# Performance work log

Measured on AMD Instinct MI355X. Metric: run time of the kernel, lower is better.

The kernel has to match this reference:

```python
import jax, jax.numpy as jnp
import numpy as np

B, TE, TD, D = 32, 2048, 64, 1024

def setup_inputs() -> dict:
    key = jax.random.key(0)
    k1, k2, k3, k4, k5 = jax.random.split(key, 5)
    return {
        "encoder_outputs": jax.random.normal(k1, (B, TE, D), dtype=jnp.float32),
        "decoder_outputs": jax.random.normal(k2, (B, TD, D), dtype=jnp.float32),
        "W_a": jax.random.normal(k3, (D, D), dtype=jnp.float32) * (1.0 / np.sqrt(D)),
        "U_a": jax.random.normal(k4, (D, D), dtype=jnp.float32) * (1.0 / np.sqrt(D)),
        "V_a": jax.random.normal(k5, (D, 1), dtype=jnp.float32) * (1.0 / np.sqrt(D)),
    }

def reference(encoder_outputs, decoder_outputs, W_a, U_a, V_a):
    # Bahdanau additive attention over encoder positions, query = last decoder step.
    dec_last = decoder_outputs[:, -1, :]                      # [B, D]
    enc_W = jnp.einsum('bte,ef->btf', encoder_outputs, W_a)   # [B, Te, D]
    dec_U = jnp.einsum('bd,df->bf', dec_last, U_a)            # [B, D] (broadcast over Te instead of tile)
    tanh_out = jnp.tanh(enc_W + dec_U[:, None, :])            # [B, Te, D]
    scores = jnp.einsum('btf,fo->bt', tanh_out, V_a[:, 0:1])  # [B, Te] (squeeze of [B,Te,1])
    weights = jax.nn.softmax(scores, axis=1)                  # [B, Te]
    context = jnp.einsum('bte,bt->be', encoder_outputs, weights)  # [B, D]
    return context, weights[..., None]
```

## Files before the change

kernel.cpp:

```cpp
#include <hip/hip_runtime.h>
#include <stdint.h>

typedef __attribute__((ext_vector_type(8))) __bf16 bf16x8;
typedef __attribute__((ext_vector_type(4))) float  f32x4;

__device__ __forceinline__ uint16_t f2b(float f) {
  uint32_t u = __float_as_uint(f);
  u += 0x7fffu + ((u >> 16) & 1u);
  return (uint16_t)(u >> 16);
}
__device__ __forceinline__ float b2f_lo(uint32_t p) { return __uint_as_float(p << 16); }
__device__ __forceinline__ float b2f_hi(uint32_t p) { return __uint_as_float(p & 0xffff0000u); }

__device__ __forceinline__ float tanh_fast(float x) {
  float e = __expf(2.0f * x);
  return 1.0f - 2.0f / (e + 1.0f);
}

__device__ __forceinline__ void barrier_lgkm() {
  asm volatile("s_waitcnt lgkmcnt(0)\n\ts_barrier" ::: "memory");
}

__global__ __launch_bounds__(256) void convert_enc(const float4* __restrict__ in,
                                                   uint4* __restrict__ out) {
  int i = blockIdx.x * 256 + threadIdx.x;
  float4 a = in[2 * i], b = in[2 * i + 1];
  uint4 o;
  o.x = (uint32_t)f2b(a.x) | ((uint32_t)f2b(a.y) << 16);
  o.y = (uint32_t)f2b(a.z) | ((uint32_t)f2b(a.w) << 16);
  o.z = (uint32_t)f2b(b.x) | ((uint32_t)f2b(b.y) << 16);
  o.w = (uint32_t)f2b(b.z) | ((uint32_t)f2b(b.w) << 16);
  out[i] = o;
}

__global__ __launch_bounds__(256) void convert_WT(const float* __restrict__ W,
                                                  uint16_t* __restrict__ WT) {
  __shared__ float tile[64][65];
  int k0 = (blockIdx.x & 15) * 64;
  int n0 = (blockIdx.x >> 4) * 64;
  #pragma unroll
  for (int it = 0; it < 16; ++it) {
    int idx = it * 256 + threadIdx.x;
    int kr = idx >> 6, nc = idx & 63;
    tile[kr][nc] = W[(size_t)(k0 + kr) * 1024 + n0 + nc];
  }
  __syncthreads();
  #pragma unroll
  for (int it = 0; it < 16; ++it) {
    int idx = it * 256 + threadIdx.x;
    int nr = idx >> 6, kc = idx & 63;
    WT[(size_t)(n0 + nr) * 1024 + k0 + kc] = f2b(tile[kc][nr]);
  }
}

__global__ __launch_bounds__(256) void compute_u(const float* __restrict__ dec,
                                                 const float4* __restrict__ U4,
                                                 float* __restrict__ u) {
  int b = blockIdx.x >> 3, dseg = blockIdx.x & 7;
  __shared__ float sdec[128];
  if (threadIdx.x < 128)
    sdec[threadIdx.x] = dec[(size_t)b * 64 * 1024 + 63 * 1024 + dseg * 128 + threadIdx.x];
  __syncthreads();
  float4 a = {0.f, 0.f, 0.f, 0.f};
  const float4* Ub = U4 + (size_t)dseg * 128 * 256 + threadIdx.x;
  #pragma unroll 4
  for (int d = 0; d < 128; ++d) {
    float4 w = Ub[(size_t)d * 256];
    float s = sdec[d];
    a.x = fmaf(s, w.x, a.x);
    a.y = fmaf(s, w.y, a.y);
    a.z = fmaf(s, w.z, a.z);
    a.w = fmaf(s, w.w, a.w);
  }
  float* up = u + b * 1024 + threadIdx.x * 4;
  atomicAdd(up + 0, a.x);
  atomicAdd(up + 1, a.y);
  atomicAdd(up + 2, a.z);
  atomicAdd(up + 3, a.w);
}

__global__ __launch_bounds__(256, 3) void gemm_score(const uint16_t* __restrict__ A,
                                                     const uint16_t* __restrict__ BT,
                                                     const float* __restrict__ u,
                                                     const float* __restrict__ v,
                                                     float* __restrict__ spart) {
  __shared__ uint4 sAB[2][1024];
  __shared__ float sred[128];

  int bx = blockIdx.x;
  int g = bx >> 6, r = bx & 63;
  int mtile = g * 8 + (r & 7);
  int ntile = r >> 3;

  int tid = threadIdx.x;
  int lane = tid & 63;
  int wid  = tid >> 6;
  int wm = (wid & 1) * 64;
  int wn = (wid >> 1) * 64;
  int quad = lane >> 4, nib = lane & 15;
  const int lsw = lane ^ ((lane >> 4) << 1);

  f32x4 acc[4][4];
  #pragma unroll
  for (int i = 0; i < 4; ++i)
    #pragma unroll
    for (int j = 0; j < 4; ++j) acc[i][j] = (f32x4){0.f, 0.f, 0.f, 0.f};

  const int rowA = mtile * 128;
  const int rowB = ntile * 128;
  const int c0 = tid, c1 = tid + 256;
  const uint4* pA0 = (const uint4*)(A  + (size_t)(rowA + (c0 >> 2)) * 1024 + (c0 & 3) * 8);
  const uint4* pA1 = (const uint4*)(A  + (size_t)(rowA + (c1 >> 2)) * 1024 + (c1 & 3) * 8);
  const uint4* pB0 = (const uint4*)(BT + (size_t)(rowB + (c0 >> 2)) * 1024 + (c0 & 3) * 8);
  const uint4* pB1 = (const uint4*)(BT + (size_t)(rowB + (c1 >> 2)) * 1024 + (c1 & 3) * 8);
  const int s0 = (((c0 >> 6) << 6) | ((c0 & 3) << 4) | ((c0 >> 2) & 15)) ^ ((c0 & 3) << 1);
  const int s1 = (((c1 >> 6) << 6) | ((c1 & 3) << 4) | ((c1 >> 2) & 15)) ^ ((c1 & 3) << 1);

  uint4 A0a, A1a, B0a, B1a, A0b, A1b, B0b, B1b;

#define GEMM_STEP(BUF)                                                          \
  do {                                                                          \
    bf16x8 af[4], bf[4];                                                        \
    _Pragma("unroll")                                                           \
    for (int i = 0; i < 4; ++i)                                                 \
      af[i] = *(const bf16x8*)&sAB[BUF][((wm >> 4) + i) * 64 + lsw];            \
    _Pragma("unroll")                                                           \
    for (int j = 0; j < 4; ++j)                                                 \
      bf[j] = *(const bf16x8*)&sAB[BUF][512 + ((wn >> 4) + j) * 64 + lsw];      \
    _Pragma("unroll")                                                           \
    for (int i = 0; i < 4; ++i)                                                 \
      _Pragma("unroll")                                                         \
      for (int j = 0; j < 4; ++j)                                               \
        acc[i][j] = __builtin_amdgcn_mfma_f32_16x16x32_bf16(af[i], bf[j],       \
                                                            acc[i][j], 0, 0, 0);\
  } while (0)

  A0a = pA0[0]; A1a = pA1[0]; B0a = pB0[0]; B1a = pB1[0];
  A0b = pA0[4]; A1b = pA1[4]; B0b = pB0[4]; B1b = pB1[4];
  sAB[0][s0] = A0a; sAB[0][s1] = A1a;
  sAB[0][512 + s0] = B0a; sAB[0][512 + s1] = B1a;
  barrier_lgkm();

  for (int k = 0; k < 32; k += 2) {
    if (k < 30) {
      A0a = pA0[(k + 2) * 4]; A1a = pA1[(k + 2) * 4];
      B0a = pB0[(k + 2) * 4]; B1a = pB1[(k + 2) * 4];
    }
    GEMM_STEP(0);
    sAB[1][s0] = A0b; sAB[1][s1] = A1b;
    sAB[1][512 + s0] = B0b; sAB[1][512 + s1] = B1b;
    barrier_lgkm();

    if (k < 29) {
      A0b = pA0[(k + 3) * 4]; A1b = pA1[(k + 3) * 4];
      B0b = pB0[(k + 3) * 4]; B1b = pB1[(k + 3) * 4];
    }
    GEMM_STEP(1);
    if (k < 30) {
      sAB[0][s0] = A0a; sAB[0][s1] = A1a;
      sAB[0][512 + s0] = B0a; sAB[0][512 + s1] = B1a;
    }
    barrier_lgkm();
  }
#undef GEMM_STEP

  int b = rowA >> 11;
  float vv[4], uu[4];
  #pragma unroll
  for (int j = 0; j < 4; ++j) {
    int col = ntile * 128 + wn + j * 16 + nib;
    vv[j] = v[col];
    uu[j] = u[b * 1024 + col];
  }
  float sloc[4][4];
  #pragma unroll
  for (int i = 0; i < 4; ++i) {
    #pragma unroll
    for (int reg = 0; reg < 4; ++reg) {
      float s = 0.f;
      #pragma unroll
      for (int j = 0; j < 4; ++j) s += vv[j] * tanh_fast(acc[i][j][reg] + uu[j]);
      s += __shfl_xor(s, 1);
      s += __shfl_xor(s, 2);
      s += __shfl_xor(s, 4);
      s += __shfl_xor(s, 8);
      sloc[i][reg] = s;
    }
  }
  if (wid < 2 && nib == 0) {
    #pragma unroll
    for (int i = 0; i < 4; ++i)
      #pragma unroll
      for (int reg = 0; reg < 4; ++reg)
        sred[wm + i * 16 + quad * 4 + reg] = sloc[i][reg];
  }
  __syncthreads();
  if (wid >= 2 && nib == 0) {
    float* outp = spart + (size_t)ntile * 65536 + rowA;
    #pragma unroll
    for (int i = 0; i < 4; ++i) {
      int rloc = wm + i * 16 + quad * 4;
      float4 sv;
      #pragma unroll
      for (int reg = 0; reg < 4; ++reg)
        ((float*)&sv)[reg] = sloc[i][reg] + sred[rloc + reg];
      *(float4*)(outp + rloc) = sv;
    }
  }
}

__global__ __launch_bounds__(256) void softmax_k(const float* __restrict__ spart,
                                                 float* __restrict__ wout) {
  int b = blockIdx.x, tid = threadIdx.x;
  __shared__ float red[4];
  float sv[8];
  float mx = -1e30f;
  #pragma unroll
  for (int i = 0; i < 8; ++i) {
    int idx = b * 2048 + i * 256 + tid;
    float s = 0.f;
    #pragma unroll
    for (int j = 0; j < 8; ++j) s += spart[j * 65536 + idx];
    sv[i] = s;
    mx = fmaxf(mx, s);
  }
  #pragma unroll
  for (int off = 1; off < 64; off <<= 1) mx = fmaxf(mx, __shfl_xor(mx, off));
  if ((tid & 63) == 0) red[tid >> 6] = mx;
  __syncthreads();
  mx = fmaxf(fmaxf(red[0], red[1]), fmaxf(red[2], red[3]));
  __syncthreads();
  float sum = 0.f;
  #pragma unroll
  for (int i = 0; i < 8; ++i) {
    sv[i] = __expf(sv[i] - mx);
    sum += sv[i];
  }
  #pragma unroll
  for (int off = 1; off < 64; off <<= 1) sum += __shfl_xor(sum, off);
  if ((tid & 63) == 0) red[tid >> 6] = sum;
  __syncthreads();
  float inv = 1.0f / (red[0] + red[1] + red[2] + red[3]);
  #pragma unroll
  for (int i = 0; i < 8; ++i) wout[b * 2048 + i * 256 + tid] = sv[i] * inv;
}

__global__ __launch_bounds__(256) void context_k(const uint16_t* __restrict__ encA,
                                                 const float* __restrict__ w,
                                                 float* __restrict__ ctx) {
  int b = blockIdx.x >> 5, ch = blockIdx.x & 31;
  int t0 = ch * 64;
  __shared__ float lw[64];
  if (threadIdx.x < 64) lw[threadIdx.x] = w[b * 2048 + t0 + threadIdx.x];
  __syncthreads();
  int e0 = threadIdx.x * 4;
  float a0 = 0.f, a1 = 0.f, a2 = 0.f, a3 = 0.f;
  const uint16_t* base = encA + (size_t)b * 2048 * 1024 + (size_t)t0 * 1024 + e0;
  #pragma unroll 4
  for (int t = 0; t < 64; ++t) {
    uint2 p = *(const uint2*)(base + (size_t)t * 1024);
    float wt = lw[t];
    a0 = fmaf(wt, b2f_lo(p.x), a0);
    a1 = fmaf(wt, b2f_hi(p.x), a1);
    a2 = fmaf(wt, b2f_lo(p.y), a2);
    a3 = fmaf(wt, b2f_hi(p.y), a3);
  }
  atomicAdd(&ctx[b * 1024 + e0 + 0], a0);
  atomicAdd(&ctx[b * 1024 + e0 + 1], a1);
  atomicAdd(&ctx[b * 1024 + e0 + 2], a2);
  atomicAdd(&ctx[b * 1024 + e0 + 3], a3);
}

extern "C" void kernel_launch(void* const* d_in, const int* in_sizes, int n_in,
                              void* d_out, int out_size, void* d_ws, size_t ws_size,
                              hipStream_t stream) {
  const float* enc = (const float*)d_in[0];
  const float* dec = (const float*)d_in[1];
  const float* Wa  = (const float*)d_in[2];
  const float* Ua  = (const float*)d_in[3];
  const float* Va  = (const float*)d_in[4];

  float* out = (float*)d_out;
  float* ctx = out;
  float* wts = out + 32 * 1024;

  char* ws = (char*)d_ws;
  uint16_t* encA  = (uint16_t*)ws;
  uint16_t* WT    = (uint16_t*)(ws + 134217728);
  float*    ub    = (float*)  (ws + 136314880);
  float*    spart = (float*)  (ws + 136445952);

  hipMemsetAsync(ctx, 0, 32 * 1024 * sizeof(float), stream);
  hipMemsetAsync(ub, 0, 32 * 1024 * sizeof(float), stream);

  convert_enc<<<32768, 256, 0, stream>>>((const float4*)enc, (uint4*)encA);
  convert_WT<<<256, 256, 0, stream>>>(Wa, WT);
  compute_u<<<256, 256, 0, stream>>>(dec, (const float4*)Ua, ub);
  gemm_score<<<4096, 256, 0, stream>>>(encA, WT, ub, Va, spart);
  softmax_k<<<32, 256, 0, stream>>>(spart, wts);
  context_k<<<1024, 256, 0, stream>>>(encA, wts, ctx);
}
```

Before: 603.1 us.

## Rewrite score GEMM with 256x256 tiles and direct global-to-LDS loads

The score GEMM moves from 128x128 tiles with 256 threads to 256x256 tiles with 512 threads (8 waves, each computing 128x64). Operands are staged straight from global memory into LDS with global_load_lds under an XOR swizzle, double-buffered, with MFMA priority raised via s_setprio. The larger tile halves the partial-score slices from 8 to 4 and raises operand reuse, which cuts global and L2 traffic. The cost is higher register pressure from 32 accumulators per thread, more LDS (128 KB of staging buffers), and fewer blocks in flight.

```diff
diff --git a/kernel.cpp b/kernel.cpp
--- a/kernel.cpp
+++ b/kernel.cpp
@@ -17,8 +17,13 @@
   return 1.0f - 2.0f / (e + 1.0f);
 }
 
-__device__ __forceinline__ void barrier_lgkm() {
-  asm volatile("s_waitcnt lgkmcnt(0)\n\ts_barrier" ::: "memory");
+__device__ __forceinline__ void bar() { asm volatile("s_barrier" ::: "memory"); }
+__device__ __forceinline__ void wait_vm0() { asm volatile("s_waitcnt vmcnt(0)" ::: "memory"); }
+
+__device__ __forceinline__ void gload16(const void* g, void* l) {
+  __builtin_amdgcn_global_load_lds(
+      (__attribute__((address_space(1))) uint32_t*)g,
+      (__attribute__((address_space(3))) uint32_t*)l, 16, 0, 0);
 }
 
 __global__ __launch_bounds__(256) void convert_enc(const float4* __restrict__ in,
@@ -79,133 +84,126 @@
   atomicAdd(up + 3, a.w);
 }
 
-__global__ __launch_bounds__(256, 3) void gemm_score(const uint16_t* __restrict__ A,
+__global__ __launch_bounds__(512, 2) void gemm_score(const uint16_t* __restrict__ A,
                                                      const uint16_t* __restrict__ BT,
                                                      const float* __restrict__ u,
                                                      const float* __restrict__ v,
                                                      float* __restrict__ spart) {
-  __shared__ uint4 sAB[2][1024];
-  __shared__ float sred[128];
-
-  int bx = blockIdx.x;
-  int g = bx >> 6, r = bx & 63;
-  int mtile = g * 8 + (r & 7);
-  int ntile = r >> 3;
-
-  int tid = threadIdx.x;
-  int lane = tid & 63;
-  int wid  = tid >> 6;
-  int wm = (wid & 1) * 64;
-  int wn = (wid >> 1) * 64;
-  int quad = lane >> 4, nib = lane & 15;
-  const int lsw = lane ^ ((lane >> 4) << 1);
-
-  f32x4 acc[4][4];
-  #pragma unroll
-  for (int i = 0; i < 4; ++i)
+  __shared__ uint4 lds4[2][4][1024];
+  __shared__ float sred[4][256];
+
+  const int bx = blockIdx.x;
+  const int wg = (bx & 7) * 128 + (bx >> 3);
+  const int mtile = wg >> 2;
+  const int ntile = wg & 3;
+
+  const int tid = threadIdx.x;
+  const int lane = tid & 63;
+  const int wid = tid >> 6;
+  const int wr = wid >> 2;
+  const int wc = wid & 3;
+  const int nib = lane & 15;
+  const int q4 = lane >> 4;
+
+  const int rowA = mtile * 256;
+  const char* baseA = (const char*)A + (size_t)rowA * 2048;
+  const char* baseB = (const char*)BT + (size_t)ntile * 256 * 2048;
+  const size_t rowoff = (size_t)(tid >> 3) * 2048 +
+                        (size_t)(((tid & 7) ^ ((tid >> 3) & 7)) << 4);
+
+#define STAGE2(nbuf, h, srcbase)                                      \
+  do {                                                                \
+    const char* _s = (srcbase);                                       \
+    gload16(_s + rowoff,             &lds4[nbuf][h][wid * 64]);       \
+    gload16(_s + rowoff + 64 * 2048, &lds4[nbuf][h][512 + wid * 64]); \
+  } while (0)
+
+  f32x4 acc[8][4];
+  #pragma unroll
+  for (int i = 0; i < 8; ++i)
     #pragma unroll
     for (int j = 0; j < 4; ++j) acc[i][j] = (f32x4){0.f, 0.f, 0.f, 0.f};
 
-  const int rowA = mtile * 128;
-  const int rowB = ntile * 128;
-  const int c0 = tid, c1 = tid + 256;
-  const uint4* pA0 = (const uint4*)(A  + (size_t)(rowA + (c0 >> 2)) * 1024 + (c0 & 3) * 8);
-  const uint4* pA1 = (const uint4*)(A  + (size_t)(rowA + (c1 >> 2)) * 1024 + (c1 & 3) * 8);
-  const uint4* pB0 = (const uint4*)(BT + (size_t)(rowB + (c0 >> 2)) * 1024 + (c0 & 3) * 8);
-  const uint4* pB1 = (const uint4*)(BT + (size_t)(rowB + (c1 >> 2)) * 1024 + (c1 & 3) * 8);
-  const int s0 = (((c0 >> 6) << 6) | ((c0 & 3) << 4) | ((c0 >> 2) & 15)) ^ ((c0 & 3) << 1);
-  const int s1 = (((c1 >> 6) << 6) | ((c1 & 3) << 4) | ((c1 >> 2) & 15)) ^ ((c1 & 3) << 1);
-
-  uint4 A0a, A1a, B0a, B1a, A0b, A1b, B0b, B1b;
-
-#define GEMM_STEP(BUF)                                                          \
-  do {                                                                          \
-    bf16x8 af[4], bf[4];                                                        \
-    _Pragma("unroll")                                                           \
-    for (int i = 0; i < 4; ++i)                                                 \
-      af[i] = *(const bf16x8*)&sAB[BUF][((wm >> 4) + i) * 64 + lsw];            \
-    _Pragma("unroll")                                                           \
-    for (int j = 0; j < 4; ++j)                                                 \
-      bf[j] = *(const bf16x8*)&sAB[BUF][512 + ((wn >> 4) + j) * 64 + lsw];      \
-    _Pragma("unroll")                                                           \
-    for (int i = 0; i < 4; ++i)                                                 \
-      _Pragma("unroll")                                                         \
-      for (int j = 0; j < 4; ++j)                                               \
-        acc[i][j] = __builtin_amdgcn_mfma_f32_16x16x32_bf16(af[i], bf[j],       \
-                                                            acc[i][j], 0, 0, 0);\
-  } while (0)
-
-  A0a = pA0[0]; A1a = pA1[0]; B0a = pB0[0]; B1a = pB1[0];
-  A0b = pA0[4]; A1b = pA1[4]; B0b = pB0[4]; B1b = pB1[4];
-  sAB[0][s0] = A0a; sAB[0][s1] = A1a;
-  sAB[0][512 + s0] = B0a; sAB[0][512 + s1] = B1a;
-  barrier_lgkm();
-
-  for (int k = 0; k < 32; k += 2) {
-    if (k < 30) {
-      A0a = pA0[(k + 2) * 4]; A1a = pA1[(k + 2) * 4];
-      B0a = pB0[(k + 2) * 4]; B1a = pB1[(k + 2) * 4];
+  STAGE2(0, 0, baseA);
+  STAGE2(0, 1, baseA + 128 * 2048);
+  STAGE2(0, 2, baseB);
+  STAGE2(0, 3, baseB + 128 * 2048);
+  wait_vm0();
+  bar();
+
+  bf16x8 bfr[4];
+  const int bhalf = 2 + (wc >> 1);
+  const int ncol0 = (wc & 1) * 64;
+
+  #pragma unroll 2
+  for (int kt = 0; kt < 16; ++kt) {
+    const int cb = kt & 1, nb = cb ^ 1;
+    const char* nA = baseA + (size_t)(kt + 1) * 128;
+    const char* nB = baseB + (size_t)(kt + 1) * 128;
+    #pragma unroll
+    for (int q = 0; q < 4; ++q) {
+      const int qi = q & 1, kk = q >> 1;
+      const int kx = (kk * 4 + q4) ^ (nib & 7);
+      bf16x8 af[4];
+      #pragma unroll
+      for (int i = 0; i < 4; ++i)
+        af[i] = *(const bf16x8*)&lds4[cb][wr][(qi * 64 + i * 16 + nib) * 8 + kx];
+      if (qi == 0) {
+        #pragma unroll
+        for (int j = 0; j < 4; ++j)
+          bfr[j] = *(const bf16x8*)&lds4[cb][bhalf][(ncol0 + j * 16 + nib) * 8 + kx];
+      }
+      if (kt < 15) {
+        if (q == 0) {
+          STAGE2(nb, 0, nA);
+          STAGE2(nb, 1, nA + 128 * 2048);
+        } else if (q == 1) {
+          STAGE2(nb, 2, nB);
+          STAGE2(nb, 3, nB + 128 * 2048);
+        }
+      }
+      bar();
+      __builtin_amdgcn_s_setprio(1);
+      #pragma unroll
+      for (int i = 0; i < 4; ++i)
+        #pragma unroll
+        for (int j = 0; j < 4; ++j)
+          acc[qi * 4 + i][j] = __builtin_amdgcn_mfma_f32_16x16x32_bf16(
+              af[i], bfr[j], acc[qi * 4 + i][j], 0, 0, 0);
+      __builtin_amdgcn_s_setprio(0);
+      if (q == 3) wait_vm0();
+      bar();
     }
-    GEMM_STEP(0);
-    sAB[1][s0] = A0b; sAB[1][s1] = A1b;
-    sAB[1][512 + s0] = B0b; sAB[1][512 + s1] = B1b;
-    barrier_lgkm();
-
-    if (k < 29) {
-      A0b = pA0[(k + 3) * 4]; A1b = pA1[(k + 3) * 4];
-      B0b = pB0[(k + 3) * 4]; B1b = pB1[(k + 3) * 4];
-    }
-    GEMM_STEP(1);
-    if (k < 30) {
-      sAB[0][s0] = A0a; sAB[0][s1] = A1a;
-      sAB[0][512 + s0] = B0a; sAB[0][512 + s1] = B1a;
-    }
-    barrier_lgkm();
-  }
-#undef GEMM_STEP
-
-  int b = rowA >> 11;
+  }
+#undef STAGE2
+
+  const int b = mtile >> 3;
   float vv[4], uu[4];
   #pragma unroll
   for (int j = 0; j < 4; ++j) {
-    int col = ntile * 128 + wn + j * 16 + nib;
+    int col = ntile * 256 + wc * 64 + j * 16 + nib;
     vv[j] = v[col];
     uu[j] = u[b * 1024 + col];
   }
-  float sloc[4][4];
-  #pragma unroll
-  for (int i = 0; i < 4; ++i) {
-    #pragma unroll
-    for (int reg = 0; reg < 4; ++reg) {
-      float s = 0.f;
-      #pragma unroll
-      for (int j = 0; j < 4; ++j) s += vv[j] * tanh_fast(acc[i][j][reg] + uu[j]);
-      s += __shfl_xor(s, 1);
-      s += __shfl_xor(s, 2);
-      s += __shfl_xor(s, 4);
-      s += __shfl_xor(s, 8);
-      sloc[i][reg] = s;
-    }
-  }
-  if (wid < 2 && nib == 0) {
+  #pragma unroll
+  for (int qi = 0; qi < 2; ++qi)
     #pragma unroll
     for (int i = 0; i < 4; ++i)
       #pragma unroll
-      for (int reg = 0; reg < 4; ++reg)
-        sred[wm + i * 16 + quad * 4 + reg] = sloc[i][reg];
-  }
-  __syncthreads();
-  if (wid >= 2 && nib == 0) {
-    float* outp = spart + (size_t)ntile * 65536 + rowA;
-    #pragma unroll
-    for (int i = 0; i < 4; ++i) {
-      int rloc = wm + i * 16 + quad * 4;
-      float4 sv;
-      #pragma unroll
-      for (int reg = 0; reg < 4; ++reg)
-        ((float*)&sv)[reg] = sloc[i][reg] + sred[rloc + reg];
-      *(float4*)(outp + rloc) = sv;
-    }
+      for (int reg = 0; reg < 4; ++reg) {
+        float s = 0.f;
+        #pragma unroll
+        for (int j = 0; j < 4; ++j) s += vv[j] * tanh_fast(acc[qi * 4 + i][j][reg] + uu[j]);
+        s += __shfl_xor(s, 1);
+        s += __shfl_xor(s, 2);
+        s += __shfl_xor(s, 4);
+        s += __shfl_xor(s, 8);
+        if (nib == 0) sred[wc][wr * 128 + qi * 64 + i * 16 + q4 * 4 + reg] = s;
+      }
+  __syncthreads();
+  if (tid < 256) {
+    float s = sred[0][tid] + sred[1][tid] + sred[2][tid] + sred[3][tid];
+    spart[(size_t)ntile * 65536 + rowA + tid] = s;
   }
 }
 
@@ -220,7 +218,7 @@
     int idx = b * 2048 + i * 256 + tid;
     float s = 0.f;
     #pragma unroll
-    for (int j = 0; j < 8; ++j) s += spart[j * 65536 + idx];
+    for (int j = 0; j < 4; ++j) s += spart[j * 65536 + idx];
     sv[i] = s;
     mx = fmaxf(mx, s);
   }
@@ -296,7 +294,7 @@
   convert_enc<<<32768, 256, 0, stream>>>((const float4*)enc, (uint4*)encA);
   convert_WT<<<256, 256, 0, stream>>>(Wa, WT);
   compute_u<<<256, 256, 0, stream>>>(dec, (const float4*)Ua, ub);
-  gemm_score<<<4096, 256, 0, stream>>>(encA, WT, ub, Va, spart);
+  gemm_score<<<1024, 512, 0, stream>>>(encA, WT, ub, Va, spart);
   softmax_k<<<32, 256, 0, stream>>>(spart, wts);
   context_k<<<1024, 256, 0, stream>>>(encA, wts, ctx);
 }
```

Result: slower. 623.2 us (+3.3%).

## Fuse encoder bf16 conversion into GEMM A-load and restructure context reduction

Applied to the files above, without the earlier changes.

Removes the separate convert_enc pass: gemm_score now reads fp32 encoder rows directly, packs them to bf16 with v_cvt_pk_bf16_f32 before staging into LDS, and the ntile==0 blocks also write the bf16 copy for the context kernel. The W transpose and u computation are merged into one prep launch. The context stage swaps atomics plus a memset for per-chunk partial sums followed by a small reduction kernel. In exchange the GEMM A loads double in bytes and add conversion work to the inner loop, and cpart reuses the spart buffer after softmax has consumed it.

```diff
diff --git a/kernel.cpp b/kernel.cpp
--- a/kernel.cpp
+++ b/kernel.cpp
@@ -12,6 +12,12 @@
 __device__ __forceinline__ float b2f_lo(uint32_t p) { return __uint_as_float(p << 16); }
 __device__ __forceinline__ float b2f_hi(uint32_t p) { return __uint_as_float(p & 0xffff0000u); }
 
+__device__ __forceinline__ uint32_t cvtpk(float lo, float hi) {
+  uint32_t r;
+  asm("v_cvt_pk_bf16_f32 %0, %1, %2" : "=v"(r) : "v"(lo), "v"(hi));
+  return r;
+}
+
 __device__ __forceinline__ float tanh_fast(float x) {
   float e = __expf(2.0f * x);
   return 1.0f - 2.0f / (e + 1.0f);
@@ -21,69 +27,60 @@
   asm volatile("s_waitcnt lgkmcnt(0)\n\ts_barrier" ::: "memory");
 }
 
-__global__ __launch_bounds__(256) void convert_enc(const float4* __restrict__ in,
-                                                   uint4* __restrict__ out) {
-  int i = blockIdx.x * 256 + threadIdx.x;
-  float4 a = in[2 * i], b = in[2 * i + 1];
-  uint4 o;
-  o.x = (uint32_t)f2b(a.x) | ((uint32_t)f2b(a.y) << 16);
-  o.y = (uint32_t)f2b(a.z) | ((uint32_t)f2b(a.w) << 16);
-  o.z = (uint32_t)f2b(b.x) | ((uint32_t)f2b(b.y) << 16);
-  o.w = (uint32_t)f2b(b.z) | ((uint32_t)f2b(b.w) << 16);
-  out[i] = o;
-}
-
-__global__ __launch_bounds__(256) void convert_WT(const float* __restrict__ W,
-                                                  uint16_t* __restrict__ WT) {
+__global__ __launch_bounds__(256) void prep(const float* __restrict__ W,
+                                            uint16_t* __restrict__ WT,
+                                            const float* __restrict__ dec,
+                                            const float4* __restrict__ U4,
+                                            float* __restrict__ u) {
   __shared__ float tile[64][65];
-  int k0 = (blockIdx.x & 15) * 64;
-  int n0 = (blockIdx.x >> 4) * 64;
-  #pragma unroll
-  for (int it = 0; it < 16; ++it) {
-    int idx = it * 256 + threadIdx.x;
-    int kr = idx >> 6, nc = idx & 63;
-    tile[kr][nc] = W[(size_t)(k0 + kr) * 1024 + n0 + nc];
-  }
-  __syncthreads();
-  #pragma unroll
-  for (int it = 0; it < 16; ++it) {
-    int idx = it * 256 + threadIdx.x;
-    int nr = idx >> 6, kc = idx & 63;
-    WT[(size_t)(n0 + nr) * 1024 + k0 + kc] = f2b(tile[kc][nr]);
-  }
-}
-
-__global__ __launch_bounds__(256) void compute_u(const float* __restrict__ dec,
-                                                 const float4* __restrict__ U4,
-                                                 float* __restrict__ u) {
-  int b = blockIdx.x >> 3, dseg = blockIdx.x & 7;
-  __shared__ float sdec[128];
-  if (threadIdx.x < 128)
-    sdec[threadIdx.x] = dec[(size_t)b * 64 * 1024 + 63 * 1024 + dseg * 128 + threadIdx.x];
-  __syncthreads();
-  float4 a = {0.f, 0.f, 0.f, 0.f};
-  const float4* Ub = U4 + (size_t)dseg * 128 * 256 + threadIdx.x;
-  #pragma unroll 4
-  for (int d = 0; d < 128; ++d) {
-    float4 w = Ub[(size_t)d * 256];
-    float s = sdec[d];
-    a.x = fmaf(s, w.x, a.x);
-    a.y = fmaf(s, w.y, a.y);
-    a.z = fmaf(s, w.z, a.z);
-    a.w = fmaf(s, w.w, a.w);
-  }
-  float* up = u + b * 1024 + threadIdx.x * 4;
-  atomicAdd(up + 0, a.x);
-  atomicAdd(up + 1, a.y);
-  atomicAdd(up + 2, a.z);
-  atomicAdd(up + 3, a.w);
-}
-
-__global__ __launch_bounds__(256, 3) void gemm_score(const uint16_t* __restrict__ A,
+  if (blockIdx.x < 256) {
+    int k0 = (blockIdx.x & 15) * 64;
+    int n0 = (blockIdx.x >> 4) * 64;
+    #pragma unroll
+    for (int it = 0; it < 16; ++it) {
+      int idx = it * 256 + threadIdx.x;
+      int kr = idx >> 6, nc = idx & 63;
+      tile[kr][nc] = W[(size_t)(k0 + kr) * 1024 + n0 + nc];
+    }
+    __syncthreads();
+    #pragma unroll
+    for (int it = 0; it < 16; ++it) {
+      int idx = it * 256 + threadIdx.x;
+      int nr = idx >> 6, kc = idx & 63;
+      WT[(size_t)(n0 + nr) * 1024 + k0 + kc] = f2b(tile[kc][nr]);
+    }
+  } else {
+    int bx = blockIdx.x - 256;
+    int b = bx >> 3, dseg = bx & 7;
+    float* sdec = &tile[0][0];
+    if (threadIdx.x < 128)
+      sdec[threadIdx.x] = dec[(size_t)b * 64 * 1024 + 63 * 1024 + dseg * 128 + threadIdx.x];
+    __syncthreads();
+    float4 a = {0.f, 0.f, 0.f, 0.f};
+    const float4* Ub = U4 + (size_t)dseg * 128 * 256 + threadIdx.x;
+    #pragma unroll 4
+    for (int d = 0; d < 128; ++d) {
+      float4 w = Ub[(size_t)d * 256];
+      float s = sdec[d];
+      a.x = fmaf(s, w.x, a.x);
+      a.y = fmaf(s, w.y, a.y);
+      a.z = fmaf(s, w.z, a.z);
+      a.w = fmaf(s, w.w, a.w);
+    }
+    float* up = u + b * 1024 + threadIdx.x * 4;
+    atomicAdd(up + 0, a.x);
+    atomicAdd(up + 1, a.y);
+    atomicAdd(up + 2, a.z);
+    atomicAdd(up + 3, a.w);
+  }
+}
+
+__global__ __launch_bounds__(256, 3) void gemm_score(const float* __restrict__ Af,
                                                      const uint16_t* __restrict__ BT,
                                                      const float* __restrict__ u,
                                                      const float* __restrict__ v,
-                                                     float* __restrict__ spart) {
+                                                     float* __restrict__ spart,
+                                                     uint16_t* __restrict__ encA) {
   __shared__ uint4 sAB[2][1024];
   __shared__ float sred[128];
 
@@ -109,14 +106,39 @@
   const int rowA = mtile * 128;
   const int rowB = ntile * 128;
   const int c0 = tid, c1 = tid + 256;
-  const uint4* pA0 = (const uint4*)(A  + (size_t)(rowA + (c0 >> 2)) * 1024 + (c0 & 3) * 8);
-  const uint4* pA1 = (const uint4*)(A  + (size_t)(rowA + (c1 >> 2)) * 1024 + (c1 & 3) * 8);
+  const float* pA0 = Af + (size_t)(rowA + (c0 >> 2)) * 1024 + (c0 & 3) * 8;
+  const float* pA1 = Af + (size_t)(rowA + (c1 >> 2)) * 1024 + (c1 & 3) * 8;
   const uint4* pB0 = (const uint4*)(BT + (size_t)(rowB + (c0 >> 2)) * 1024 + (c0 & 3) * 8);
   const uint4* pB1 = (const uint4*)(BT + (size_t)(rowB + (c1 >> 2)) * 1024 + (c1 & 3) * 8);
+  uint16_t* eb0 = encA + (size_t)(rowA + (c0 >> 2)) * 1024 + (c0 & 3) * 8;
+  uint16_t* eb1 = encA + (size_t)(rowA + (c1 >> 2)) * 1024 + (c1 & 3) * 8;
+  const bool doexp = (ntile == 0);
   const int s0 = (((c0 >> 6) << 6) | ((c0 & 3) << 4) | ((c0 >> 2) & 15)) ^ ((c0 & 3) << 1);
   const int s1 = (((c1 >> 6) << 6) | ((c1 & 3) << 4) | ((c1 >> 2) & 15)) ^ ((c1 & 3) << 1);
 
-  uint4 A0a, A1a, B0a, B1a, A0b, A1b, B0b, B1b;
+  float4 A0aL, A0aH, A1aL, A1aH, A0bL, A0bH, A1bL, A1bH;
+  uint4 B0a, B1a, B0b, B1b;
+
+#define LDA(L, H, P, K)                                  \
+  do {                                                   \
+    L = *(const float4*)((P) + (K) * 32);                \
+    H = *(const float4*)((P) + (K) * 32 + 4);            \
+  } while (0)
+
+#define STAGEA(BUF, SK, A0L, A0H, A1L, A1H, B0, B1)                      \
+  do {                                                                   \
+    uint4 p0, p1;                                                        \
+    p0.x = cvtpk(A0L.x, A0L.y); p0.y = cvtpk(A0L.z, A0L.w);              \
+    p0.z = cvtpk(A0H.x, A0H.y); p0.w = cvtpk(A0H.z, A0H.w);              \
+    p1.x = cvtpk(A1L.x, A1L.y); p1.y = cvtpk(A1L.z, A1L.w);              \
+    p1.z = cvtpk(A1H.x, A1H.y); p1.w = cvtpk(A1H.z, A1H.w);              \
+    sAB[BUF][s0] = p0; sAB[BUF][s1] = p1;                                \
+    sAB[BUF][512 + s0] = B0; sAB[BUF][512 + s1] = B1;                    \
+    if (doexp) {                                                         \
+      *(uint4*)(eb0 + (SK) * 32) = p0;                                   \
+      *(uint4*)(eb1 + (SK) * 32) = p1;                                   \
+    }                                                                    \
+  } while (0)
 
 #define GEMM_STEP(BUF)                                                          \
   do {                                                                          \
@@ -135,34 +157,35 @@
                                                             acc[i][j], 0, 0, 0);\
   } while (0)
 
-  A0a = pA0[0]; A1a = pA1[0]; B0a = pB0[0]; B1a = pB1[0];
-  A0b = pA0[4]; A1b = pA1[4]; B0b = pB0[4]; B1b = pB1[4];
-  sAB[0][s0] = A0a; sAB[0][s1] = A1a;
-  sAB[0][512 + s0] = B0a; sAB[0][512 + s1] = B1a;
+  LDA(A0aL, A0aH, pA0, 0); LDA(A1aL, A1aH, pA1, 0);
+  B0a = pB0[0]; B1a = pB1[0];
+  LDA(A0bL, A0bH, pA0, 1); LDA(A1bL, A1bH, pA1, 1);
+  B0b = pB0[4]; B1b = pB1[4];
+  STAGEA(0, 0, A0aL, A0aH, A1aL, A1aH, B0a, B1a);
   barrier_lgkm();
 
   for (int k = 0; k < 32; k += 2) {
     if (k < 30) {
-      A0a = pA0[(k + 2) * 4]; A1a = pA1[(k + 2) * 4];
+      LDA(A0aL, A0aH, pA0, k + 2); LDA(A1aL, A1aH, pA1, k + 2);
       B0a = pB0[(k + 2) * 4]; B1a = pB1[(k + 2) * 4];
     }
     GEMM_STEP(0);
-    sAB[1][s0] = A0b; sAB[1][s1] = A1b;
-    sAB[1][512 + s0] = B0b; sAB[1][512 + s1] = B1b;
+    STAGEA(1, k + 1, A0bL, A0bH, A1bL, A1bH, B0b, B1b);
     barrier_lgkm();
 
     if (k < 29) {
-      A0b = pA0[(k + 3) * 4]; A1b = pA1[(k + 3) * 4];
+      LDA(A0bL, A0bH, pA0, k + 3); LDA(A1bL, A1bH, pA1, k + 3);
       B0b = pB0[(k + 3) * 4]; B1b = pB1[(k + 3) * 4];
     }
     GEMM_STEP(1);
     if (k < 30) {
-      sAB[0][s0] = A0a; sAB[0][s1] = A1a;
-      sAB[0][512 + s0] = B0a; sAB[0][512 + s1] = B1a;
+      STAGEA(0, k + 2, A0aL, A0aH, A1aL, A1aH, B0a, B1a);
     }
     barrier_lgkm();
   }
 #undef GEMM_STEP
+#undef STAGEA
+#undef LDA
 
   int b = rowA >> 11;
   float vv[4], uu[4];
@@ -245,30 +268,59 @@
   for (int i = 0; i < 8; ++i) wout[b * 2048 + i * 256 + tid] = sv[i] * inv;
 }
 
-__global__ __launch_bounds__(256) void context_k(const uint16_t* __restrict__ encA,
-                                                 const float* __restrict__ w,
-                                                 float* __restrict__ ctx) {
-  int b = blockIdx.x >> 5, ch = blockIdx.x & 31;
-  int t0 = ch * 64;
-  __shared__ float lw[64];
-  if (threadIdx.x < 64) lw[threadIdx.x] = w[b * 2048 + t0 + threadIdx.x];
-  __syncthreads();
-  int e0 = threadIdx.x * 4;
-  float a0 = 0.f, a1 = 0.f, a2 = 0.f, a3 = 0.f;
-  const uint16_t* base = encA + (size_t)b * 2048 * 1024 + (size_t)t0 * 1024 + e0;
-  #pragma unroll 4
+__global__ __launch_bounds__(256) void context_part(const uint16_t* __restrict__ encA,
+                                                    const float* __restrict__ w,
+                                                    float* __restrict__ cpart) {
+  int b = blockIdx.x >> 4, ch = blockIdx.x & 15;
+  int t0 = ch * 128;
+  __shared__ float lw[128];
+  __shared__ float sctx[1024];
+  if (threadIdx.x < 128) lw[threadIdx.x] = w[b * 2048 + t0 + threadIdx.x];
+  __syncthreads();
+  int th = threadIdx.x >> 7;
+  int i  = threadIdx.x & 127;
+  int e0 = i * 8;
+  float a[8] = {0.f, 0.f, 0.f, 0.f, 0.f, 0.f, 0.f, 0.f};
+  const uint16_t* base = encA + (size_t)b * 2048 * 1024 + (size_t)(t0 + th * 64) * 1024 + e0;
+  const float* lwp = lw + th * 64;
+  #pragma unroll 2
   for (int t = 0; t < 64; ++t) {
-    uint2 p = *(const uint2*)(base + (size_t)t * 1024);
-    float wt = lw[t];
-    a0 = fmaf(wt, b2f_lo(p.x), a0);
-    a1 = fmaf(wt, b2f_hi(p.x), a1);
-    a2 = fmaf(wt, b2f_lo(p.y), a2);
-    a3 = fmaf(wt, b2f_hi(p.y), a3);
-  }
-  atomicAdd(&ctx[b * 1024 + e0 + 0], a0);
-  atomicAdd(&ctx[b * 1024 + e0 + 1], a1);
-  atomicAdd(&ctx[b * 1024 + e0 + 2], a2);
-  atomicAdd(&ctx[b * 1024 + e0 + 3], a3);
+    uint4 p = *(const uint4*)(base + (size_t)t * 1024);
+    float wt = lwp[t];
+    a[0] = fmaf(wt, b2f_lo(p.x), a[0]);
+    a[1] = fmaf(wt, b2f_hi(p.x), a[1]);
+    a[2] = fmaf(wt, b2f_lo(p.y), a[2]);
+    a[3] = fmaf(wt, b2f_hi(p.y), a[3]);
+    a[4] = fmaf(wt, b2f_lo(p.z), a[4]);
+    a[5] = fmaf(wt, b2f_hi(p.z), a[5]);
+    a[6] = fmaf(wt, b2f_lo(p.w), a[6]);
+    a[7] = fmaf(wt, b2f_hi(p.w), a[7]);
+  }
+  if (th == 0) {
+    #pragma unroll
+    for (int k = 0; k < 8; ++k) sctx[e0 + k] = a[k];
+  }
+  __syncthreads();
+  if (th == 1) {
+    float* cp = cpart + (size_t)(b * 16 + ch) * 1024 + e0;
+    float4 v0, v1;
+    #pragma unroll
+    for (int k = 0; k < 4; ++k) ((float*)&v0)[k] = a[k] + sctx[e0 + k];
+    #pragma unroll
+    for (int k = 0; k < 4; ++k) ((float*)&v1)[k] = a[4 + k] + sctx[e0 + 4 + k];
+    *(float4*)(cp) = v0;
+    *(float4*)(cp + 4) = v1;
+  }
+}
+
+__global__ __launch_bounds__(256) void ctx_reduce(const float* __restrict__ cpart,
+                                                  float* __restrict__ ctx) {
+  int idx = blockIdx.x * 256 + threadIdx.x;
+  int b = idx >> 10, e = idx & 1023;
+  float s = 0.f;
+  #pragma unroll
+  for (int r = 0; r < 16; ++r) s += cpart[(size_t)(b * 16 + r) * 1024 + e];
+  ctx[idx] = s;
 }
 
 extern "C" void kernel_launch(void* const* d_in, const int* in_sizes, int n_in,
@@ -289,14 +341,13 @@
   uint16_t* WT    = (uint16_t*)(ws + 134217728);
   float*    ub    = (float*)  (ws + 136314880);
   float*    spart = (float*)  (ws + 136445952);
-
-  hipMemsetAsync(ctx, 0, 32 * 1024 * sizeof(float), stream);
+  float*    cpart = spart;
+
   hipMemsetAsync(ub, 0, 32 * 1024 * sizeof(float), stream);
 
-  convert_enc<<<32768, 256, 0, stream>>>((const float4*)enc, (uint4*)encA);
-  convert_WT<<<256, 256, 0, stream>>>(Wa, WT);
-  compute_u<<<256, 256, 0, stream>>>(dec, (const float4*)Ua, ub);
-  gemm_score<<<4096, 256, 0, stream>>>(encA, WT, ub, Va, spart);
+  prep<<<512, 256, 0, stream>>>(Wa, WT, dec, (const float4*)Ua, ub);
+  gemm_score<<<4096, 256, 0, stream>>>(enc, WT, ub, Va, spart, encA);
   softmax_k<<<32, 256, 0, stream>>>(spart, wts);
-  context_k<<<1024, 256, 0, stream>>>(encA, wts, ctx);
-}
+  context_part<<<512, 256, 0, stream>>>(encA, wts, cpart);
+  ctx_reduce<<<128, 256, 0, stream>>>(cpart, ctx);
+}
```

Result: slower. 728.4 us (+20.8%).

## Fuse prep kernels and memsets into one launch; fuse softmax into context

Applied to the files above, without the earlier changes.

Merges the encoder conversion, W transpose, U projection and ctx zeroing into a single block-indexed prep kernel, so the two memsets and two launches go away and the u atomics become a direct store. Softmax is recomputed redundantly in each of 16 blocks per batch, which then compute their slice of the context with wider 16-byte loads, a shared-memory pair reduction and fewer atomics. This cuts launch count and the round-trip of the weights through global memory. In exchange, the U projection now runs on only 32 blocks, each looping over all 1024 rows, and every context block re-reads the full score partials.

```diff
diff --git a/kernel.cpp b/kernel.cpp
--- a/kernel.cpp
+++ b/kernel.cpp
@@ -21,62 +21,64 @@
   asm volatile("s_waitcnt lgkmcnt(0)\n\ts_barrier" ::: "memory");
 }
 
-__global__ __launch_bounds__(256) void convert_enc(const float4* __restrict__ in,
-                                                   uint4* __restrict__ out) {
-  int i = blockIdx.x * 256 + threadIdx.x;
-  float4 a = in[2 * i], b = in[2 * i + 1];
-  uint4 o;
-  o.x = (uint32_t)f2b(a.x) | ((uint32_t)f2b(a.y) << 16);
-  o.y = (uint32_t)f2b(a.z) | ((uint32_t)f2b(a.w) << 16);
-  o.z = (uint32_t)f2b(b.x) | ((uint32_t)f2b(b.y) << 16);
-  o.w = (uint32_t)f2b(b.z) | ((uint32_t)f2b(b.w) << 16);
-  out[i] = o;
-}
-
-__global__ __launch_bounds__(256) void convert_WT(const float* __restrict__ W,
-                                                  uint16_t* __restrict__ WT) {
+__global__ __launch_bounds__(256) void prep(const float4* __restrict__ enc4,
+                                            uint4* __restrict__ encA4,
+                                            const float* __restrict__ W,
+                                            uint16_t* __restrict__ WT,
+                                            const float* __restrict__ dec,
+                                            const float4* __restrict__ U4,
+                                            float* __restrict__ u,
+                                            float* __restrict__ ctx) {
   __shared__ float tile[64][65];
-  int k0 = (blockIdx.x & 15) * 64;
-  int n0 = (blockIdx.x >> 4) * 64;
-  #pragma unroll
-  for (int it = 0; it < 16; ++it) {
-    int idx = it * 256 + threadIdx.x;
-    int kr = idx >> 6, nc = idx & 63;
-    tile[kr][nc] = W[(size_t)(k0 + kr) * 1024 + n0 + nc];
-  }
-  __syncthreads();
-  #pragma unroll
-  for (int it = 0; it < 16; ++it) {
-    int idx = it * 256 + threadIdx.x;
-    int nr = idx >> 6, kc = idx & 63;
-    WT[(size_t)(n0 + nr) * 1024 + k0 + kc] = f2b(tile[kc][nr]);
-  }
-}
-
-__global__ __launch_bounds__(256) void compute_u(const float* __restrict__ dec,
-                                                 const float4* __restrict__ U4,
-                                                 float* __restrict__ u) {
-  int b = blockIdx.x >> 3, dseg = blockIdx.x & 7;
-  __shared__ float sdec[128];
-  if (threadIdx.x < 128)
-    sdec[threadIdx.x] = dec[(size_t)b * 64 * 1024 + 63 * 1024 + dseg * 128 + threadIdx.x];
-  __syncthreads();
-  float4 a = {0.f, 0.f, 0.f, 0.f};
-  const float4* Ub = U4 + (size_t)dseg * 128 * 256 + threadIdx.x;
-  #pragma unroll 4
-  for (int d = 0; d < 128; ++d) {
-    float4 w = Ub[(size_t)d * 256];
-    float s = sdec[d];
-    a.x = fmaf(s, w.x, a.x);
-    a.y = fmaf(s, w.y, a.y);
-    a.z = fmaf(s, w.z, a.z);
-    a.w = fmaf(s, w.w, a.w);
-  }
-  float* up = u + b * 1024 + threadIdx.x * 4;
-  atomicAdd(up + 0, a.x);
-  atomicAdd(up + 1, a.y);
-  atomicAdd(up + 2, a.z);
-  atomicAdd(up + 3, a.w);
+  const int bx = blockIdx.x;
+  const int tid = threadIdx.x;
+  if (bx < 32) {
+    int b = bx;
+    float* sdec = &tile[0][0];
+    ((float4*)sdec)[tid] = *((const float4*)(dec + (size_t)b * 65536 + 64512) + tid);
+    __syncthreads();
+    float4 a = {0.f, 0.f, 0.f, 0.f};
+    const float4* Ub = U4 + tid;
+    #pragma unroll 4
+    for (int d = 0; d < 1024; ++d) {
+      float4 w = Ub[(size_t)d * 256];
+      float s = sdec[d];
+      a.x = fmaf(s, w.x, a.x);
+      a.y = fmaf(s, w.y, a.y);
+      a.z = fmaf(s, w.z, a.z);
+      a.w = fmaf(s, w.w, a.w);
+    }
+    *(float4*)(u + b * 1024 + tid * 4) = a;
+  } else if (bx < 288) {
+    int bxl = bx - 32;
+    int k0 = (bxl & 15) * 64;
+    int n0 = (bxl >> 4) * 64;
+    #pragma unroll
+    for (int it = 0; it < 16; ++it) {
+      int idx = it * 256 + tid;
+      int kr = idx >> 6, nc = idx & 63;
+      tile[kr][nc] = W[(size_t)(k0 + kr) * 1024 + n0 + nc];
+    }
+    __syncthreads();
+    #pragma unroll
+    for (int it = 0; it < 16; ++it) {
+      int idx = it * 256 + tid;
+      int nr = idx >> 6, kc = idx & 63;
+      WT[(size_t)(n0 + nr) * 1024 + k0 + kc] = f2b(tile[kc][nr]);
+    }
+  } else if (bx < 320) {
+    float4 z = {0.f, 0.f, 0.f, 0.f};
+    *(float4*)(ctx + (size_t)((bx - 288) * 256 + tid) * 4) = z;
+  } else {
+    int i = (bx - 320) * 256 + tid;
+    float4 a = enc4[2 * i], b = enc4[2 * i + 1];
+    uint4 o;
+    o.x = (uint32_t)f2b(a.x) | ((uint32_t)f2b(a.y) << 16);
+    o.y = (uint32_t)f2b(a.z) | ((uint32_t)f2b(a.w) << 16);
+    o.z = (uint32_t)f2b(b.x) | ((uint32_t)f2b(b.y) << 16);
+    o.w = (uint32_t)f2b(b.z) | ((uint32_t)f2b(b.w) << 16);
+    encA4[i] = o;
+  }
 }
 
 __global__ __launch_bounds__(256, 3) void gemm_score(const uint16_t* __restrict__ A,
@@ -209,10 +211,16 @@
   }
 }
 
-__global__ __launch_bounds__(256) void softmax_k(const float* __restrict__ spart,
-                                                 float* __restrict__ wout) {
-  int b = blockIdx.x, tid = threadIdx.x;
+__global__ __launch_bounds__(256) void ctx_softmax(const float* __restrict__ spart,
+                                                   const uint16_t* __restrict__ encA,
+                                                   float* __restrict__ wts,
+                                                   float* __restrict__ ctx) {
+  int b = blockIdx.x >> 4, ch = blockIdx.x & 15;
+  int tid = threadIdx.x;
+  __shared__ float lw[2048];
+  __shared__ float sctx[1024];
   __shared__ float red[4];
+
   float sv[8];
   float mx = -1e30f;
   #pragma unroll
@@ -242,33 +250,43 @@
   __syncthreads();
   float inv = 1.0f / (red[0] + red[1] + red[2] + red[3]);
   #pragma unroll
-  for (int i = 0; i < 8; ++i) wout[b * 2048 + i * 256 + tid] = sv[i] * inv;
-}
-
-__global__ __launch_bounds__(256) void context_k(const uint16_t* __restrict__ encA,
-                                                 const float* __restrict__ w,
-                                                 float* __restrict__ ctx) {
-  int b = blockIdx.x >> 5, ch = blockIdx.x & 31;
-  int t0 = ch * 64;
-  __shared__ float lw[64];
-  if (threadIdx.x < 64) lw[threadIdx.x] = w[b * 2048 + t0 + threadIdx.x];
-  __syncthreads();
-  int e0 = threadIdx.x * 4;
-  float a0 = 0.f, a1 = 0.f, a2 = 0.f, a3 = 0.f;
-  const uint16_t* base = encA + (size_t)b * 2048 * 1024 + (size_t)t0 * 1024 + e0;
-  #pragma unroll 4
+  for (int i = 0; i < 8; ++i) {
+    float wv = sv[i] * inv;
+    lw[i * 256 + tid] = wv;
+    if (ch == 0) wts[b * 2048 + i * 256 + tid] = wv;
+  }
+  __syncthreads();
+
+  int th = tid >> 7;
+  int ig = tid & 127;
+  int e0 = ig * 8;
+  float a[8] = {0.f, 0.f, 0.f, 0.f, 0.f, 0.f, 0.f, 0.f};
+  const uint16_t* base = encA + (size_t)b * 2048 * 1024 +
+                         (size_t)(ch * 128 + th * 64) * 1024 + e0;
+  const float* lwp = lw + ch * 128 + th * 64;
+  #pragma unroll 2
   for (int t = 0; t < 64; ++t) {
-    uint2 p = *(const uint2*)(base + (size_t)t * 1024);
-    float wt = lw[t];
-    a0 = fmaf(wt, b2f_lo(p.x), a0);
-    a1 = fmaf(wt, b2f_hi(p.x), a1);
-    a2 = fmaf(wt, b2f_lo(p.y), a2);
-    a3 = fmaf(wt, b2f_hi(p.y), a3);
-  }
-  atomicAdd(&ctx[b * 1024 + e0 + 0], a0);
-  atomicAdd(&ctx[b * 1024 + e0 + 1], a1);
-  atomicAdd(&ctx[b * 1024 + e0 + 2], a2);
-  atomicAdd(&ctx[b * 1024 + e0 + 3], a3);
+    uint4 p = *(const uint4*)(base + (size_t)t * 1024);
+    float wt = lwp[t];
+    a[0] = fmaf(wt, b2f_lo(p.x), a[0]);
+    a[1] = fmaf(wt, b2f_hi(p.x), a[1]);
+    a[2] = fmaf(wt, b2f_lo(p.y), a[2]);
+    a[3] = fmaf(wt, b2f_hi(p.y), a[3]);
+    a[4] = fmaf(wt, b2f_lo(p.z), a[4]);
+    a[5] = fmaf(wt, b2f_hi(p.z), a[5]);
+    a[6] = fmaf(wt, b2f_lo(p.w), a[6]);
+    a[7] = fmaf(wt, b2f_hi(p.w), a[7]);
+  }
+  if (th == 0) {
+    #pragma unroll
+    for (int k = 0; k < 8; ++k) sctx[e0 + k] = a[k];
+  }
+  __syncthreads();
+  if (th == 1) {
+    float* cp = ctx + b * 1024 + e0;
+    #pragma unroll
+    for (int k = 0; k < 8; ++k) atomicAdd(cp + k, a[k] + sctx[e0 + k]);
+  }
 }
 
 extern "C" void kernel_launch(void* const* d_in, const int* in_sizes, int n_in,
@@ -290,13 +308,8 @@
   float*    ub    = (float*)  (ws + 136314880);
   float*    spart = (float*)  (ws + 136445952);
 
-  hipMemsetAsync(ctx, 0, 32 * 1024 * sizeof(float), stream);
-  hipMemsetAsync(ub, 0, 32 * 1024 * sizeof(float), stream);
-
-  convert_enc<<<32768, 256, 0, stream>>>((const float4*)enc, (uint4*)encA);
-  convert_WT<<<256, 256, 0, stream>>>(Wa, WT);
-  compute_u<<<256, 256, 0, stream>>>(dec, (const float4*)Ua, ub);
+  prep<<<33088, 256, 0, stream>>>((const float4*)enc, (uint4*)encA, Wa, WT,
+                                  dec, (const float4*)Ua, ub, ctx);
   gemm_score<<<4096, 256, 0, stream>>>(encA, WT, ub, Va, spart);
-  softmax_k<<<32, 256, 0, stream>>>(spart, wts);
-  context_k<<<1024, 256, 0, stream>>>(encA, wts, ctx);
-}
+  ctx_softmax<<<512, 256, 0, stream>>>(spart, encA, wts, ctx);
+}
```

New measurement: 673.4 us. 11.7% more time.
